# Performance work log

Hardware: AMD Instinct MI355X
Metric: run time of the kernel (lower is better)

Reference implementation:

```python
import jax, jax.numpy as jnp
import numpy as np

IN_F, OUT_F = 512, 512
GRID_SIZE, SPLINE_ORDER = 5, 3
K = GRID_SIZE + SPLINE_ORDER  # 8 basis functions
B, S = 8, 1024


def setup_inputs() -> dict:
    key = jax.random.key(0)
    k1, k2, k3, k4, k5 = jax.random.split(key, 5)
    return {
        "x": jax.random.normal(k1, (B, S, IN_F), dtype=jnp.float32),
        "coeff": jax.random.normal(k2, (OUT_F, IN_F, K), dtype=jnp.float32),
        "scale_base": jax.random.normal(k3, (OUT_F, IN_F), dtype=jnp.float32) * 0.1,
        "scale_spline": jax.random.normal(k4, (OUT_F, IN_F), dtype=jnp.float32),
        "base_bias": jax.random.normal(k5, (OUT_F, IN_F), dtype=jnp.float32),
    }


def reference(x, coeff, scale_base, scale_spline, base_bias):
    batch = x.shape[0]
    in_f = x.shape[-1]
    k = coeff.shape[-1]

    xc = jnp.clip(x.reshape(-1, in_f), -1.0, 1.0)      # (N, in)
    base = jax.nn.silu(xc)                              # (N, in)

    # polynomial basis recurrence: b0 = 1, b1 = x, b_i = 2*x*b_{i-1} - 1
    bases = [jnp.ones_like(xc), xc]
    for _ in range(2, k):
        bases.append(2.0 * xc * bases[-1] - 1.0)
    basis = jnp.stack(bases[:k], axis=-1)               # (N, in, K)

    # spline[n,o] = sum_{i,k} scale_spline[o,i]*coeff[o,i,k]*basis[n,i,k]
    w_spline = scale_spline[..., None] * coeff          # (out, in, K)
    spline_term = jnp.einsum('nik,oik->no', basis, w_spline)
    base_term = base @ scale_base.T                     # (N, out)
    out = base_term + spline_term + jnp.sum(base_bias, axis=1)  # (N, out)

    out = out.reshape(batch, -1, base_bias.shape[0])    # (B, S, out)
    if out.shape[-2] == 1:
        out = out[..., 0, :]
    return out
```

## Files before the change

### kernel.cpp

```cpp
#include <hip/hip_runtime.h>
#include <hip/hip_bf16.h>

#define IN_FEAT 512
#define OUT_FEAT 512
#define NTOK 8192
#define KDIM 4096

typedef short bf16x8 __attribute__((ext_vector_type(8)));
typedef float f32x4 __attribute__((ext_vector_type(4)));
typedef float f32x16 __attribute__((ext_vector_type(16)));

static __device__ inline short f2bf(float f) {
    union { float f; unsigned u; } v; v.f = f;
    unsigned u = v.u;
    u += 0x7fffu + ((u >> 16) & 1u);
    return (short)(u >> 16);
}

static __device__ inline unsigned pack2bf(float f0, float f1) {
    union { float f; unsigned u; } a, b; a.f = f0; b.f = f1;
    return __builtin_amdgcn_perm(b.u + 0x8000u, a.u + 0x8000u, 0x07060302u);
}

static __device__ inline bf16x8 gen_chunk(float xv) {
    float xc = fminf(fmaxf(xv, -1.f), 1.f);
    float e  = __expf(-xc);
    float bse = xc * __builtin_amdgcn_rcpf(1.f + e);
    float b2 = 2.f * xc * xc - 1.f;
    float b3 = 2.f * xc * b2 - 1.f;
    float b4 = 2.f * xc * b3 - 1.f;
    float b5 = 2.f * xc * b4 - 1.f;
    float b6 = 2.f * xc * b5 - 1.f;
    float b7 = 2.f * xc * b6 - 1.f;
    union { uint4 u; bf16x8 v; } r;
    r.u.x = pack2bf(bse, xc);
    r.u.y = pack2bf(b2, b3);
    r.u.z = pack2bf(b4, b5);
    r.u.w = pack2bf(b6, b7);
    return r.v;
}

static __device__ inline void gload_lds16(const short* g, short* l) {
    __builtin_amdgcn_global_load_lds(
        (const __attribute__((address_space(1))) unsigned int*)g,
        (__attribute__((address_space(3))) unsigned int*)l,
        16, 0, 0);
}

__global__ __launch_bounds__(256) void kan_prep(
    const float* __restrict__ coeff, const float* __restrict__ scale_base,
    const float* __restrict__ scale_spline, const float* __restrict__ base_bias,
    short* __restrict__ Wb, float* __restrict__ bias)
{
    int o = blockIdx.x;
    int tid = threadIdx.x;
    float local = 0.f;
#pragma unroll
    for (int rep = 0; rep < 2; ++rep) {
        int i = tid + rep * 256;
        size_t oi = (size_t)o * IN_FEAT + i;
        const float4* c4 = (const float4*)(coeff + oi * 8);
        float4 ca = c4[0], cb = c4[1];
        float ss = scale_spline[oi];
        float sb = scale_base[oi];
        local += base_bias[oi] + ss * ca.x;
        bf16x8 w;
        w[0] = f2bf(sb);
        w[1] = f2bf(ss * ca.y); w[2] = f2bf(ss * ca.z); w[3] = f2bf(ss * ca.w);
        w[4] = f2bf(ss * cb.x); w[5] = f2bf(ss * cb.y); w[6] = f2bf(ss * cb.z);
        w[7] = f2bf(ss * cb.w);
        *(bf16x8*)(Wb + (size_t)o * KDIM + (size_t)i * 8) = w;
    }
    __shared__ float red[4];
    for (int off = 32; off > 0; off >>= 1) local += __shfl_down(local, off, 64);
    int lane = tid & 63, wv = tid >> 6;
    if (lane == 0) red[wv] = local;
    __syncthreads();
    if (tid == 0) bias[o] = red[0] + red[1] + red[2] + red[3];
}

#define RSTR 67

__global__ __launch_bounds__(256, 2) void kan_gemm9(
    const float* __restrict__ x, const short* __restrict__ Wb,
    const float* __restrict__ bias, float* __restrict__ out)
{
    __shared__ __align__(16) short Bs[2][2][128 * 64];
    __shared__ __align__(16) float xsl[2][16 * 64];

    int tid = threadIdx.x;
    int nb = blockIdx.x & 3;
    int mb = blockIdx.x >> 2;
    int m0 = mb * 64, o0 = nb * 128;

    int lane = tid & 63, wv = tid >> 6;
    int wn = wv & 1, kk = wv >> 1;
    int l31 = lane & 31, half = lane >> 5;

    f32x16 acc[2][2];
#pragma unroll
    for (int a = 0; a < 2; ++a)
#pragma unroll
        for (int b = 0; b < 2; ++b) acc[a][b] = (f32x16)0.f;

    int rg = lane >> 3;
    int c_log = (lane & 7) ^ rg;
    const short* Bg0 = Wb + (size_t)(o0 + wv * 32 + rg) * KDIM + c_log * 8;
    const short* Bg1 = Bg0 + 2048;

    int xrow = tid >> 2, p = tid & 3;
    int xh = p >> 1, xq = p & 1;
    const float* xg = x + (size_t)(m0 + xrow) * IN_FEAT + xh * 256 + xq * 4;
    int sbase = (xh * 8 + xq * 4) * 64 + xrow;

#define STAGE(buf, it)                                                        \
    {                                                                         \
        const short* b0_ = Bg0 + (it) * 64;                                   \
        const short* b1_ = Bg1 + (it) * 64;                                   \
        _Pragma("unroll")                                                     \
        for (int j = 0; j < 4; ++j) {                                         \
            gload_lds16(b0_ + (size_t)j * 8 * KDIM, &Bs[buf][0][(wv * 32 + j * 8) * 64]); \
            gload_lds16(b1_ + (size_t)j * 8 * KDIM, &Bs[buf][1][(wv * 32 + j * 8) * 64]); \
        }                                                                     \
        float4 v_ = *(const float4*)(xg + (it) * 8);                          \
        xsl[buf][sbase]       = v_.x;                                         \
        xsl[buf][sbase + 64]  = v_.y;                                         \
        xsl[buf][sbase + 128] = v_.z;                                         \
        xsl[buf][sbase + 192] = v_.w;                                         \
    }

    STAGE(0, 0);
    int cur = 0;
    for (int it = 0; it < 32; ++it, cur ^= 1) {
        __syncthreads();
        if (it < 31) { int nxt = cur ^ 1; STAGE(nxt, it + 1); }
#pragma unroll
        for (int istep = 0; istep < 4; ++istep) {
            int clog = istep * 2 + half;
            bf16x8 bfr[2], af[2];
#pragma unroll
            for (int fn = 0; fn < 2; ++fn) {
                int row = wn * 64 + fn * 32 + l31;
                bfr[fn] = *(const bf16x8*)&Bs[cur][kk][row * 64 + (clog ^ (row & 7)) * 8];
            }
            int inp = kk * 8 + istep * 2 + half;
#pragma unroll
            for (int fm = 0; fm < 2; ++fm)
                af[fm] = gen_chunk(xsl[cur][inp * 64 + fm * 32 + l31]);
#pragma unroll
            for (int fm = 0; fm < 2; ++fm)
#pragma unroll
                for (int fn = 0; fn < 2; ++fn)
                    acc[fm][fn] = __builtin_amdgcn_mfma_f32_32x32x16_bf16(
                        af[fm], bfr[fn], acc[fm][fn], 0, 0, 0);
        }
    }
#undef STAGE

    float* rbuf = (float*)&Bs[0][0][0];
    int base = (wn * 64 + lane) * RSTR;
    __syncthreads();
    if (kk == 1) {
#pragma unroll
        for (int fm = 0; fm < 2; ++fm)
#pragma unroll
            for (int fn = 0; fn < 2; ++fn)
#pragma unroll
                for (int r = 0; r < 16; ++r)
                    rbuf[base + (fm * 2 + fn) * 16 + r] = acc[fm][fn][r];
    }
    __syncthreads();
    if (kk == 0) {
#pragma unroll
        for (int fn = 0; fn < 2; ++fn) {
            int o = o0 + wn * 64 + fn * 32 + l31;
            float bv = bias[o];
#pragma unroll
            for (int fm = 0; fm < 2; ++fm) {
#pragma unroll
                for (int r = 0; r < 16; ++r) {
                    float v = acc[fm][fn][r] + rbuf[base + (fm * 2 + fn) * 16 + r] + bv;
                    int token = m0 + fm * 32 + (r & 3) + 8 * (r >> 2) + 4 * half;
                    out[(size_t)token * OUT_FEAT + o] = v;
                }
            }
        }
    }
}

extern "C" void kernel_launch(void* const* d_in, const int* in_sizes, int n_in,
                              void* d_out, int out_size, void* d_ws, size_t ws_size,
                              hipStream_t stream) {
    const float* x            = (const float*)d_in[0];
    const float* coeff        = (const float*)d_in[1];
    const float* scale_base   = (const float*)d_in[2];
    const float* scale_spline = (const float*)d_in[3];
    const float* base_bias    = (const float*)d_in[4];
    float* out = (float*)d_out;

    short* Wb   = (short*)d_ws;
    float* bias = (float*)((char*)d_ws + (size_t)OUT_FEAT * KDIM * 2);

    kan_prep<<<OUT_FEAT, 256, 0, stream>>>(coeff, scale_base, scale_spline, base_bias, Wb, bias);
    kan_gemm9<<<(NTOK / 64) * (OUT_FEAT / 128), 256, 0, stream>>>(x, Wb, bias, out);
}
```

Before: 134.4 us.

## Halve K-step tile and shared memory to raise occupancy to four blocks per CU

Shrinks the per-iteration K slice from 64 to 32 columns (64 iterations instead of 32), cutting LDS per block roughly in half. Launch bounds are raised from 2 to 4 blocks per CU. The B-tile and x staging are rearranged so each wave pair handles a split of the smaller tile. This aims to hide load latency through more resident waves, but it doubles the number of barriers and the per-iteration overhead, and tightens the register budget.

```diff
diff --git a/kernel.cpp b/kernel.cpp
--- a/kernel.cpp
+++ b/kernel.cpp
@@ -7,7 +7,6 @@
 #define KDIM 4096
 
 typedef short bf16x8 __attribute__((ext_vector_type(8)));
-typedef float f32x4 __attribute__((ext_vector_type(4)));
 typedef float f32x16 __attribute__((ext_vector_type(16)));
 
 static __device__ inline short f2bf(float f) {
@@ -81,12 +80,13 @@
 
 #define RSTR 67
 
-__global__ __launch_bounds__(256, 2) void kan_gemm9(
+__global__ __launch_bounds__(256, 4) void kan_gemm11(
     const float* __restrict__ x, const short* __restrict__ Wb,
     const float* __restrict__ bias, float* __restrict__ out)
 {
-    __shared__ __align__(16) short Bs[2][2][128 * 64];
-    __shared__ __align__(16) float xsl[2][16 * 64];
+    __shared__ __align__(16) short POOL[18432];
+    short* Bs  = POOL;
+    float* xsl = (float*)(POOL + 16384);
 
     int tid = threadIdx.x;
     int nb = blockIdx.x & 3;
@@ -104,49 +104,47 @@
         for (int b = 0; b < 2; ++b) acc[a][b] = (f32x16)0.f;
 
     int rg = lane >> 3;
-    int c_log = (lane & 7) ^ rg;
-    const short* Bg0 = Wb + (size_t)(o0 + wv * 32 + rg) * KDIM + c_log * 8;
-    const short* Bg1 = Bg0 + 2048;
+    int g  = (lane & 7) ^ rg;
+    const short* Bg = Wb + (size_t)(o0 + wv * 32 + rg) * KDIM
+                         + (g >> 2) * 2048 + (g & 3) * 8;
 
     int xrow = tid >> 2, p = tid & 3;
     int xh = p >> 1, xq = p & 1;
-    const float* xg = x + (size_t)(m0 + xrow) * IN_FEAT + xh * 256 + xq * 4;
-    int sbase = (xh * 8 + xq * 4) * 64 + xrow;
+    const float* xg = x + (size_t)(m0 + xrow) * IN_FEAT + xh * 256 + xq * 2;
+    int sb0 = (xh * 4 + xq * 2) * 64 + xrow;
 
 #define STAGE(buf, it)                                                        \
     {                                                                         \
-        const short* b0_ = Bg0 + (it) * 64;                                   \
-        const short* b1_ = Bg1 + (it) * 64;                                   \
+        short* bd_ = Bs + (buf) * 8192 + wv * 2048;                           \
+        const short* bg_ = Bg + (size_t)(it) * 32;                            \
         _Pragma("unroll")                                                     \
-        for (int j = 0; j < 4; ++j) {                                         \
-            gload_lds16(b0_ + (size_t)j * 8 * KDIM, &Bs[buf][0][(wv * 32 + j * 8) * 64]); \
-            gload_lds16(b1_ + (size_t)j * 8 * KDIM, &Bs[buf][1][(wv * 32 + j * 8) * 64]); \
-        }                                                                     \
-        float4 v_ = *(const float4*)(xg + (it) * 8);                          \
-        xsl[buf][sbase]       = v_.x;                                         \
-        xsl[buf][sbase + 64]  = v_.y;                                         \
-        xsl[buf][sbase + 128] = v_.z;                                         \
-        xsl[buf][sbase + 192] = v_.w;                                         \
+        for (int j = 0; j < 4; ++j)                                           \
+            gload_lds16(bg_ + (size_t)j * 8 * KDIM, bd_ + j * 512);           \
+        float2 v_ = *(const float2*)(xg + (size_t)(it) * 4);                  \
+        float* xd_ = xsl + (buf) * 512 + sb0;                                 \
+        xd_[0]  = v_.x;                                                       \
+        xd_[64] = v_.y;                                                       \
     }
 
     STAGE(0, 0);
     int cur = 0;
-    for (int it = 0; it < 32; ++it, cur ^= 1) {
+    for (int it = 0; it < 64; ++it, cur ^= 1) {
         __syncthreads();
-        if (it < 31) { int nxt = cur ^ 1; STAGE(nxt, it + 1); }
-#pragma unroll
-        for (int istep = 0; istep < 4; ++istep) {
-            int clog = istep * 2 + half;
+        if (it < 63) { int nxt = cur ^ 1; STAGE(nxt, it + 1); }
+        const short* Bsc = Bs + cur * 8192;
+        const float* xc_ = xsl + cur * 512;
+#pragma unroll
+        for (int istep = 0; istep < 2; ++istep) {
+            int clog = kk * 4 + istep * 2 + half;
             bf16x8 bfr[2], af[2];
 #pragma unroll
             for (int fn = 0; fn < 2; ++fn) {
                 int row = wn * 64 + fn * 32 + l31;
-                bfr[fn] = *(const bf16x8*)&Bs[cur][kk][row * 64 + (clog ^ (row & 7)) * 8];
+                bfr[fn] = *(const bf16x8*)(Bsc + row * 64 + ((clog ^ (row & 7)) * 8));
             }
-            int inp = kk * 8 + istep * 2 + half;
 #pragma unroll
             for (int fm = 0; fm < 2; ++fm)
-                af[fm] = gen_chunk(xsl[cur][inp * 64 + fm * 32 + l31]);
+                af[fm] = gen_chunk(xc_[clog * 64 + fm * 32 + l31]);
 #pragma unroll
             for (int fm = 0; fm < 2; ++fm)
 #pragma unroll
@@ -157,7 +155,7 @@
     }
 #undef STAGE
 
-    float* rbuf = (float*)&Bs[0][0][0];
+    float* rbuf = (float*)POOL;
     int base = (wn * 64 + lane) * RSTR;
     __syncthreads();
     if (kk == 1) {
@@ -202,5 +200,5 @@
     float* bias = (float*)((char*)d_ws + (size_t)OUT_FEAT * KDIM * 2);
 
     kan_prep<<<OUT_FEAT, 256, 0, stream>>>(coeff, scale_base, scale_spline, base_bias, Wb, bias);
-    kan_gemm9<<<(NTOK / 64) * (OUT_FEAT / 128), 256, 0, stream>>>(x, Wb, bias, out);
-}
+    kan_gemm11<<<(NTOK / 64) * (OUT_FEAT / 128), 256, 0, stream>>>(x, Wb, bias, out);
+}
```

Result: slower. 143.1 us (+6.5%).
